# Kernel tuning notes

Hardware: AMD Instinct MI355X
Metric: run time of the kernel (lower is better)

The kernel has to match this reference:

```python
import jax, jax.numpy as jnp
import numpy as np
import math

D_MODEL = 1024
NUM_NEURONS = 2048
LUT_SIZE = 4096
TWO_PI = 2.0 * math.pi


def lut_sin_cos(theta, sin_table, cos_table):
    # Interpolated periodic table lookup over [0, 2*pi)
    n = sin_table.shape[0]
    pos = (theta / TWO_PI) * n
    pos = jnp.mod(pos, n)
    i0 = jnp.floor(pos).astype(jnp.int32)
    frac = pos - i0.astype(theta.dtype)
    i1 = jnp.mod(i0 + 1, n)
    s = sin_table[i0] * (1.0 - frac) + sin_table[i1] * frac
    c = cos_table[i0] * (1.0 - frac) + cos_table[i1] * frac
    return s, c


def setup_inputs() -> dict:
    key = jax.random.key(0)
    ks = jax.random.split(key, 10)
    B = 64
    x_real = jax.random.normal(ks[0], (B, D_MODEL), jnp.float32)
    x_imag = jax.random.normal(ks[1], (B, D_MODEL), jnp.float32)
    t = jax.random.uniform(ks[2], (B,), jnp.float32)
    # xavier_uniform with gain=0.5 for linear weights
    def xavier(k, shape, gain):
        fan_out, fan_in = shape
        a = gain * math.sqrt(6.0 / (fan_in + fan_out))
        return jax.random.uniform(k, shape, jnp.float32, -a, a)
    ic_w = xavier(ks[3], (D_MODEL, 2 * D_MODEL), 0.5)
    ic_b = jnp.zeros((D_MODEL,), jnp.float32)
    W = jax.random.normal(ks[4], (NUM_NEURONS, D_MODEL), jnp.float32) * 0.02
    Bp = jnp.zeros((NUM_NEURONS, D_MODEL), jnp.float32)
    attn_cos = jnp.ones((NUM_NEURONS, D_MODEL), jnp.float32)
    attn_sin = jnp.ones((NUM_NEURONS, D_MODEL), jnp.float32)
    wr = xavier(ks[5], (D_MODEL, NUM_NEURONS), 0.5)
    wi = xavier(ks[6], (D_MODEL, NUM_NEURONS), 0.5)
    grid = jnp.arange(LUT_SIZE, dtype=jnp.float32) * (TWO_PI / LUT_SIZE)
    sin_table = jnp.sin(grid)
    cos_table = jnp.cos(grid)
    return {"x_real": x_real, "x_imag": x_imag, "t": t,
            "ic_w": ic_w, "ic_b": ic_b, "W": W, "Bp": Bp,
            "attn_cos": attn_cos, "attn_sin": attn_sin,
            "wr": wr, "wi": wi,
            "sin_table": sin_table, "cos_table": cos_table}


def reference(x_real, x_imag, t, ic_w, ic_b, W, Bp, attn_cos, attn_sin, wr, wi, sin_table, cos_table):
    x_combined = jnp.concatenate([x_real, x_imag], axis=-1)          # [B, 2D]
    x_collapsed = x_combined @ ic_w.T + ic_b                          # [B, D]
    wavelength = 1.0 + jnp.abs(W)                                     # [N, D]
    theta = x_collapsed[:, None, :] / wavelength + Bp + t[:, None, None]  # [B, N, D]
    sin_t, cos_t = lut_sin_cos(theta, sin_table, cos_table)
    cos_sum = jnp.einsum('bnd,nd->bn', cos_t, attn_cos)               # fused weight+reduce
    sin_sum = jnp.einsum('bnd,nd->bn', sin_t, attn_sin)
    out_real = jax.nn.silu(cos_sum @ wr.T)                            # [B, D]
    out_imag = jax.nn.silu(sin_sum @ wi.T)
    return out_real, out_imag
```

## Files before the change

kernel.cpp:

```cpp
#include <hip/hip_runtime.h>
#include <stdint.h>

#define DM 1024
#define NN 2048
#define BB 64

static constexpr float INV2PI = 0.15915494309189535f;

__device__ __forceinline__ uint32_t bf16r(float x) {
  uint32_t b = __float_as_uint(x);
  b += 0x7fffu + ((b >> 16) & 1u);
  return b >> 16;
}

__global__ __launch_bounds__(256) void k0_prep(
    const float* __restrict__ xr, const float* __restrict__ xi,
    const float* __restrict__ W,
    float* __restrict__ xcombP, float* __restrict__ rinv)
{
  __shared__ float tile[64][65];
  int bid = blockIdx.x;
  int t = threadIdx.x;
  if (bid < 32) {
    int j = bid;
    int k0 = j * 64;
    const float* src = (k0 < 1024) ? xr : xi;
    int koff = k0 & 1023;
    int c = t & 63, rl = t >> 6;
#pragma unroll
    for (int i = 0; i < 16; ++i) {
      int b = rl * 16 + i;
      tile[b][c] = src[b * 1024 + koff + c];
    }
    __syncthreads();
    float2* out2 = (float2*)xcombP;
    int bl = t & 63, kp = t >> 6;
#pragma unroll
    for (int i = 0; i < 8; ++i) {
      int kl = (kp * 8 + i) * 2;
      float2 v = make_float2(tile[bl][kl], tile[bl][kl + 1]);
      out2[(size_t)((k0 + kl) >> 1) * 64 + bl] = v;
    }
  } else {
    int j = bid - 32;
    const float4* W4 = (const float4*)W;
    float4* R4 = (float4*)rinv;
    int base = j * 2048 + t;
#pragma unroll
    for (int i = 0; i < 8; ++i) {
      int idx = base + i * 256;
      float4 w = W4[idx];
      float4 r;
      r.x = 1.0f / (1.0f + fabsf(w.x));
      r.y = 1.0f / (1.0f + fabsf(w.y));
      r.z = 1.0f / (1.0f + fabsf(w.z));
      r.w = 1.0f / (1.0f + fabsf(w.w));
      R4[idx] = r;
    }
  }
}

__global__ __launch_bounds__(512) void k1_collapse(
    const float* __restrict__ xcombP, const float* __restrict__ icw,
    const float* __restrict__ icb, uint32_t* __restrict__ xcp)
{
  __shared__ float part[8][4][64];
  int d0 = blockIdx.x * 4;
  int wave = __builtin_amdgcn_readfirstlane((int)(threadIdx.x >> 6));
  int lane = threadIdx.x & 63;
  const float2* P2 = (const float2*)xcombP;
  float acc[4] = {0.f, 0.f, 0.f, 0.f};
  int kbase = wave * 256;
  for (int kk = 0; kk < 256; kk += 4) {
    int k = kbase + kk;
    float2 xa = P2[(size_t)(k >> 1) * 64 + lane];
    float2 xb = P2[(size_t)((k >> 1) + 1) * 64 + lane];
#pragma unroll
    for (int r = 0; r < 4; ++r) {
      float4 w = *(const float4*)(icw + (size_t)(d0 + r) * 2048 + k);
      acc[r] = fmaf(w.x, xa.x, acc[r]);
      acc[r] = fmaf(w.y, xa.y, acc[r]);
      acc[r] = fmaf(w.z, xb.x, acc[r]);
      acc[r] = fmaf(w.w, xb.y, acc[r]);
    }
  }
#pragma unroll
  for (int r = 0; r < 4; ++r) part[wave][r][lane] = acc[r];
  __syncthreads();
  int t = threadIdx.x;
  if (t < 128) {
    int pj = t >> 6;
    int b = t & 63;
    float s0 = 0.f, s1 = 0.f;
#pragma unroll
    for (int w = 0; w < 8; ++w) {
      s0 += part[w][2 * pj][b];
      s1 += part[w][2 * pj + 1][b];
    }
    float x0 = (s0 + icb[d0 + 2 * pj]) * INV2PI;
    float x1 = (s1 + icb[d0 + 2 * pj + 1]) * INV2PI;
    uint32_t u = bf16r(x0) | (bf16r(x1) << 16);
    xcp[(size_t)((d0 >> 1) + pj) * 64 + b] = u;
  }
}

#define K2_STEP(r4, b4, a4, s4, xu0, xu1)                                 \
  do {                                                                     \
    float x0 = __uint_as_float((xu0) << 16);                               \
    float x1 = __uint_as_float((xu0) & 0xffff0000u);                       \
    float x2 = __uint_as_float((xu1) << 16);                               \
    float x3 = __uint_as_float((xu1) & 0xffff0000u);                       \
    float rv0 = fmaf(x0, (r4).x, fmaf((b4).x, INV2PI, t2));                \
    accc0 = fmaf(__builtin_amdgcn_cosf(rv0), (a4).x, accc0);               \
    accs0 = fmaf(__builtin_amdgcn_sinf(rv0), (s4).x, accs0);               \
    float rv1 = fmaf(x1, (r4).y, fmaf((b4).y, INV2PI, t2));                \
    accc1 = fmaf(__builtin_amdgcn_cosf(rv1), (a4).y, accc1);               \
    accs1 = fmaf(__builtin_amdgcn_sinf(rv1), (s4).y, accs1);               \
    float rv2 = fmaf(x2, (r4).z, fmaf((b4).z, INV2PI, t2));                \
    accc0 = fmaf(__builtin_amdgcn_cosf(rv2), (a4).z, accc0);               \
    accs0 = fmaf(__builtin_amdgcn_sinf(rv2), (s4).z, accs0);               \
    float rv3 = fmaf(x3, (r4).w, fmaf((b4).w, INV2PI, t2));                \
    accc1 = fmaf(__builtin_amdgcn_cosf(rv3), (a4).w, accc1);               \
    accs1 = fmaf(__builtin_amdgcn_sinf(rv3), (s4).w, accs1);               \
  } while (0)

__global__ __launch_bounds__(512) void k2_resonant(
    const uint32_t* __restrict__ xcp, const float* __restrict__ rinv,
    const float* __restrict__ Bp, const float* __restrict__ ac,
    const float* __restrict__ as_, const float* __restrict__ tin,
    float* __restrict__ csP, float* __restrict__ ssP)
{
  __shared__ __align__(16) uint32_t xlds[64][64];
  __shared__ __align__(16) float plds[2][8][4][64];
  int wave = __builtin_amdgcn_readfirstlane((int)(threadIdx.x >> 6));
  int lane = threadIdx.x & 63;
  int bid = blockIdx.x;
  int q = bid & 7;
  int n = (bid >> 3) * 8 + wave;
  float t2 = tin[lane] * INV2PI;

  const char* xsrc = (const char*)(xcp + (size_t)q * 64 * 64);
  char* xdst = (char*)&xlds[0][0];
#pragma unroll
  for (int r = 0; r < 2; ++r) {
    int j = wave * 2 + r;
    __builtin_amdgcn_global_load_lds(
        (const __attribute__((address_space(1))) void*)(xsrc + j * 1024 + lane * 16),
        (__attribute__((address_space(3))) void*)(xdst + j * 1024), 16, 0, 0);
  }

  int g = lane >> 4;
  const float* ab = (g == 0) ? rinv : (g == 1) ? Bp : (g == 2) ? ac : as_;
  const float* gp = ab + (size_t)n * 1024 + (size_t)q * 128 + (lane & 15) * 4;
#pragma unroll
  for (int c = 0; c < 2; ++c) {
    __builtin_amdgcn_global_load_lds(
        (const __attribute__((address_space(1))) void*)(gp + c * 64),
        (__attribute__((address_space(3))) void*)&plds[c][wave][0][0], 16, 0, 0);
  }

  __syncthreads();

  float accc0 = 0.f, accs0 = 0.f, accc1 = 0.f, accs1 = 0.f;

#pragma unroll
  for (int c = 0; c < 2; ++c) {
    const float4* pr = (const float4*)&plds[c][wave][0][0];
#pragma unroll 4
    for (int i = 0; i < 16; ++i) {
      int ga = c * 16 + i;
      uint32_t xu0 = xlds[2 * ga][lane];
      uint32_t xu1 = xlds[2 * ga + 1][lane];
      float4 r4 = pr[i];
      float4 b4 = pr[16 + i];
      float4 a4 = pr[32 + i];
      float4 s4 = pr[48 + i];
      K2_STEP(r4, b4, a4, s4, xu0, xu1);
    }
  }

  size_t o = ((size_t)q * 2048 + n) * 64 + lane;
  csP[o] = accc0 + accc1;
  ssP[o] = accs0 + accs1;
}

__global__ __launch_bounds__(256) void k2b_reduce(
    const float* __restrict__ csP, const float* __restrict__ ssP,
    float* __restrict__ csT, float* __restrict__ ssT)
{
  int i = blockIdx.x * 256 + threadIdx.x;
  float c = 0.f, s = 0.f;
#pragma unroll
  for (int j = 0; j < 8; ++j) {
    c += csP[i + j * 131072];
    s += ssP[i + j * 131072];
  }
  csT[i] = c;
  ssT[i] = s;
}

__global__ __launch_bounds__(512) void k3_out(
    const float* __restrict__ csT, const float* __restrict__ ssT,
    const float* __restrict__ wr, const float* __restrict__ wi,
    float* __restrict__ out)
{
  __shared__ float part[8][4][65];
  int bid = blockIdx.x;
  int sel = bid >> 8;
  int d0 = (bid & 255) * 4;
  int wave = __builtin_amdgcn_readfirstlane((int)(threadIdx.x >> 6));
  int lane = threadIdx.x & 63;
  const float* src = sel ? ssT : csT;
  const float* wt = sel ? wi : wr;
  float acc[4] = {0.f, 0.f, 0.f, 0.f};
  int n0 = wave * 256;
  for (int i = 0; i < 64; ++i) {
    int n = n0 + i * 4;
    float cv0 = src[(size_t)(n + 0) * 64 + lane];
    float cv1 = src[(size_t)(n + 1) * 64 + lane];
    float cv2 = src[(size_t)(n + 2) * 64 + lane];
    float cv3 = src[(size_t)(n + 3) * 64 + lane];
#pragma unroll
    for (int r = 0; r < 4; ++r) {
      float4 wv = *(const float4*)(wt + (size_t)(d0 + r) * 2048 + n);
      acc[r] = fmaf(cv0, wv.x, acc[r]);
      acc[r] = fmaf(cv1, wv.y, acc[r]);
      acc[r] = fmaf(cv2, wv.z, acc[r]);
      acc[r] = fmaf(cv3, wv.w, acc[r]);
    }
  }
#pragma unroll
  for (int r = 0; r < 4; ++r) part[wave][r][lane] = acc[r];
  __syncthreads();
  int t = threadIdx.x;
  if (t < 256) {
    int b = t >> 2, j = t & 3;
    float s = 0.f;
#pragma unroll
    for (int w = 0; w < 8; ++w) s += part[w][j][b];
    float y = s / (1.0f + __expf(-s));
    out[(size_t)sel * 65536 + (size_t)b * 1024 + d0 + j] = y;
  }
}

extern "C" void kernel_launch(void* const* d_in, const int* in_sizes, int n_in,
                              void* d_out, int out_size, void* d_ws, size_t ws_size,
                              hipStream_t stream) {
  const float* xr  = (const float*)d_in[0];
  const float* xi  = (const float*)d_in[1];
  const float* t   = (const float*)d_in[2];
  const float* icw = (const float*)d_in[3];
  const float* icb = (const float*)d_in[4];
  const float* W   = (const float*)d_in[5];
  const float* Bp  = (const float*)d_in[6];
  const float* ac  = (const float*)d_in[7];
  const float* as_ = (const float*)d_in[8];
  const float* wr  = (const float*)d_in[9];
  const float* wi  = (const float*)d_in[10];

  float* ws = (float*)d_ws;
  float* rinv   = ws;
  float* xcombP = ws + 2097152;
  uint32_t* xcp = (uint32_t*)(ws + 2228224);
  float* csP    = ws + 2260992;
  float* ssP    = ws + 3309568;
  float* csT    = ws + 4358144;
  float* ssT    = ws + 4489216;
  float* out = (float*)d_out;

  k0_prep<<<dim3(288), dim3(256), 0, stream>>>(xr, xi, W, xcombP, rinv);
  k1_collapse<<<dim3(256), dim3(512), 0, stream>>>(xcombP, icw, icb, xcp);
  k2_resonant<<<dim3(2048), dim3(512), 0, stream>>>(xcp, rinv, Bp, ac, as_, t, csP, ssP);
  k2b_reduce<<<dim3(512), dim3(256), 0, stream>>>(csP, ssP, csT, ssT);
  k3_out<<<dim3(512), dim3(512), 0, stream>>>(csT, ssT, wr, wi, out);
}
```

Before: 78.20 us.

## Batch loads in collapse/output GEMVs, split k2 accumulators, pack reduced sums as bf16

k1_collapse and k3_out now issue 16 weight float4 loads and 8 activation loads per iteration before the FMAs, so more memory requests are in flight at once. k2_resonant is fully unrolled and uses four independent accumulator pairs, which shortens the FMA dependency chains. k2b_reduce now sums two neurons per thread and writes the results as packed bf16, halving the bytes k3_out reads for its activations. In exchange this adds bf16 rounding error on the reduced sums and raises register pressure in the unrolled loops.

```diff
diff --git a/kernel.cpp b/kernel.cpp
--- a/kernel.cpp
+++ b/kernel.cpp
@@ -71,17 +71,27 @@
   const float2* P2 = (const float2*)xcombP;
   float acc[4] = {0.f, 0.f, 0.f, 0.f};
   int kbase = wave * 256;
-  for (int kk = 0; kk < 256; kk += 4) {
+  for (int kk = 0; kk < 256; kk += 16) {
     int k = kbase + kk;
-    float2 xa = P2[(size_t)(k >> 1) * 64 + lane];
-    float2 xb = P2[(size_t)((k >> 1) + 1) * 64 + lane];
-#pragma unroll
-    for (int r = 0; r < 4; ++r) {
-      float4 w = *(const float4*)(icw + (size_t)(d0 + r) * 2048 + k);
-      acc[r] = fmaf(w.x, xa.x, acc[r]);
-      acc[r] = fmaf(w.y, xa.y, acc[r]);
-      acc[r] = fmaf(w.z, xb.x, acc[r]);
-      acc[r] = fmaf(w.w, xb.y, acc[r]);
+    float4 w[4][4];
+#pragma unroll
+    for (int r = 0; r < 4; ++r)
+#pragma unroll
+      for (int j = 0; j < 4; ++j)
+        w[r][j] = *(const float4*)(icw + (size_t)(d0 + r) * 2048 + k + 4 * j);
+    float2 xv[8];
+#pragma unroll
+    for (int j = 0; j < 8; ++j)
+      xv[j] = P2[(size_t)((k >> 1) + j) * 64 + lane];
+#pragma unroll
+    for (int j = 0; j < 4; ++j) {
+#pragma unroll
+      for (int r = 0; r < 4; ++r) {
+        acc[r] = fmaf(w[r][j].x, xv[2 * j].x, acc[r]);
+        acc[r] = fmaf(w[r][j].y, xv[2 * j].y, acc[r]);
+        acc[r] = fmaf(w[r][j].z, xv[2 * j + 1].x, acc[r]);
+        acc[r] = fmaf(w[r][j].w, xv[2 * j + 1].y, acc[r]);
+      }
     }
   }
 #pragma unroll
@@ -104,24 +114,24 @@
   }
 }
 
-#define K2_STEP(r4, b4, a4, s4, xu0, xu1)                                 \
+#define K2_STEP(r4, b4, a4, s4, xu0, xu1, AC0, AS0, AC1, AS1)              \
   do {                                                                     \
     float x0 = __uint_as_float((xu0) << 16);                               \
     float x1 = __uint_as_float((xu0) & 0xffff0000u);                       \
     float x2 = __uint_as_float((xu1) << 16);                               \
     float x3 = __uint_as_float((xu1) & 0xffff0000u);                       \
     float rv0 = fmaf(x0, (r4).x, fmaf((b4).x, INV2PI, t2));                \
-    accc0 = fmaf(__builtin_amdgcn_cosf(rv0), (a4).x, accc0);               \
-    accs0 = fmaf(__builtin_amdgcn_sinf(rv0), (s4).x, accs0);               \
+    AC0 = fmaf(__builtin_amdgcn_cosf(rv0), (a4).x, AC0);                   \
+    AS0 = fmaf(__builtin_amdgcn_sinf(rv0), (s4).x, AS0);                   \
     float rv1 = fmaf(x1, (r4).y, fmaf((b4).y, INV2PI, t2));                \
-    accc1 = fmaf(__builtin_amdgcn_cosf(rv1), (a4).y, accc1);               \
-    accs1 = fmaf(__builtin_amdgcn_sinf(rv1), (s4).y, accs1);               \
+    AC1 = fmaf(__builtin_amdgcn_cosf(rv1), (a4).y, AC1);                   \
+    AS1 = fmaf(__builtin_amdgcn_sinf(rv1), (s4).y, AS1);                   \
     float rv2 = fmaf(x2, (r4).z, fmaf((b4).z, INV2PI, t2));                \
-    accc0 = fmaf(__builtin_amdgcn_cosf(rv2), (a4).z, accc0);               \
-    accs0 = fmaf(__builtin_amdgcn_sinf(rv2), (s4).z, accs0);               \
+    AC0 = fmaf(__builtin_amdgcn_cosf(rv2), (a4).z, AC0);                   \
+    AS0 = fmaf(__builtin_amdgcn_sinf(rv2), (s4).z, AS0);                   \
     float rv3 = fmaf(x3, (r4).w, fmaf((b4).w, INV2PI, t2));                \
-    accc1 = fmaf(__builtin_amdgcn_cosf(rv3), (a4).w, accc1);               \
-    accs1 = fmaf(__builtin_amdgcn_sinf(rv3), (s4).w, accs1);               \
+    AC1 = fmaf(__builtin_amdgcn_cosf(rv3), (a4).w, AC1);                   \
+    AS1 = fmaf(__builtin_amdgcn_sinf(rv3), (s4).w, AS1);                   \
   } while (0)
 
 __global__ __launch_bounds__(512) void k2_resonant(
@@ -161,46 +171,63 @@
 
   __syncthreads();
 
-  float accc0 = 0.f, accs0 = 0.f, accc1 = 0.f, accs1 = 0.f;
-
-#pragma unroll
-  for (int c = 0; c < 2; ++c) {
-    const float4* pr = (const float4*)&plds[c][wave][0][0];
-#pragma unroll 4
+  float ac0 = 0.f, as0 = 0.f, ac1 = 0.f, as1 = 0.f;
+  float ac2 = 0.f, as2 = 0.f, ac3 = 0.f, as3 = 0.f;
+
+  {
+    const float4* pr = (const float4*)&plds[0][wave][0][0];
+#pragma unroll
     for (int i = 0; i < 16; ++i) {
-      int ga = c * 16 + i;
-      uint32_t xu0 = xlds[2 * ga][lane];
-      uint32_t xu1 = xlds[2 * ga + 1][lane];
+      uint32_t xu0 = xlds[2 * i][lane];
+      uint32_t xu1 = xlds[2 * i + 1][lane];
       float4 r4 = pr[i];
       float4 b4 = pr[16 + i];
       float4 a4 = pr[32 + i];
       float4 s4 = pr[48 + i];
-      K2_STEP(r4, b4, a4, s4, xu0, xu1);
+      K2_STEP(r4, b4, a4, s4, xu0, xu1, ac0, as0, ac1, as1);
+    }
+  }
+  {
+    const float4* pr = (const float4*)&plds[1][wave][0][0];
+#pragma unroll
+    for (int i = 0; i < 16; ++i) {
+      uint32_t xu0 = xlds[32 + 2 * i][lane];
+      uint32_t xu1 = xlds[32 + 2 * i + 1][lane];
+      float4 r4 = pr[i];
+      float4 b4 = pr[16 + i];
+      float4 a4 = pr[32 + i];
+      float4 s4 = pr[48 + i];
+      K2_STEP(r4, b4, a4, s4, xu0, xu1, ac2, as2, ac3, as3);
     }
   }
 
   size_t o = ((size_t)q * 2048 + n) * 64 + lane;
-  csP[o] = accc0 + accc1;
-  ssP[o] = accs0 + accs1;
+  csP[o] = (ac0 + ac1) + (ac2 + ac3);
+  ssP[o] = (as0 + as1) + (as2 + as3);
 }
 
 __global__ __launch_bounds__(256) void k2b_reduce(
     const float* __restrict__ csP, const float* __restrict__ ssP,
-    float* __restrict__ csT, float* __restrict__ ssT)
+    uint32_t* __restrict__ csB, uint32_t* __restrict__ ssB)
 {
   int i = blockIdx.x * 256 + threadIdx.x;
-  float c = 0.f, s = 0.f;
+  int np = i >> 6, b = i & 63;
+  int n0 = 2 * np;
+  float c0 = 0.f, c1 = 0.f, s0 = 0.f, s1 = 0.f;
 #pragma unroll
   for (int j = 0; j < 8; ++j) {
-    c += csP[i + j * 131072];
-    s += ssP[i + j * 131072];
-  }
-  csT[i] = c;
-  ssT[i] = s;
+    size_t base = ((size_t)j * 2048 + n0) * 64 + b;
+    c0 += csP[base];
+    c1 += csP[base + 64];
+    s0 += ssP[base];
+    s1 += ssP[base + 64];
+  }
+  csB[i] = bf16r(c0) | (bf16r(c1) << 16);
+  ssB[i] = bf16r(s0) | (bf16r(s1) << 16);
 }
 
 __global__ __launch_bounds__(512) void k3_out(
-    const float* __restrict__ csT, const float* __restrict__ ssT,
+    const uint32_t* __restrict__ csB, const uint32_t* __restrict__ ssB,
     const float* __restrict__ wr, const float* __restrict__ wi,
     float* __restrict__ out)
 {
@@ -210,23 +237,40 @@
   int d0 = (bid & 255) * 4;
   int wave = __builtin_amdgcn_readfirstlane((int)(threadIdx.x >> 6));
   int lane = threadIdx.x & 63;
-  const float* src = sel ? ssT : csT;
+  const uint32_t* src2 = sel ? ssB : csB;
   const float* wt = sel ? wi : wr;
   float acc[4] = {0.f, 0.f, 0.f, 0.f};
   int n0 = wave * 256;
-  for (int i = 0; i < 64; ++i) {
-    int n = n0 + i * 4;
-    float cv0 = src[(size_t)(n + 0) * 64 + lane];
-    float cv1 = src[(size_t)(n + 1) * 64 + lane];
-    float cv2 = src[(size_t)(n + 2) * 64 + lane];
-    float cv3 = src[(size_t)(n + 3) * 64 + lane];
-#pragma unroll
-    for (int r = 0; r < 4; ++r) {
-      float4 wv = *(const float4*)(wt + (size_t)(d0 + r) * 2048 + n);
-      acc[r] = fmaf(cv0, wv.x, acc[r]);
-      acc[r] = fmaf(cv1, wv.y, acc[r]);
-      acc[r] = fmaf(cv2, wv.z, acc[r]);
-      acc[r] = fmaf(cv3, wv.w, acc[r]);
+  for (int i = 0; i < 16; ++i) {
+    int n = n0 + i * 16;
+    float4 w[4][4];
+#pragma unroll
+    for (int r = 0; r < 4; ++r)
+#pragma unroll
+      for (int j = 0; j < 4; ++j)
+        w[r][j] = *(const float4*)(wt + (size_t)(d0 + r) * 2048 + n + 4 * j);
+    uint32_t xu[8];
+#pragma unroll
+    for (int j = 0; j < 8; ++j)
+      xu[j] = src2[(size_t)((n >> 1) + j) * 64 + lane];
+#pragma unroll
+    for (int j = 0; j < 8; ++j) {
+      float cv0 = __uint_as_float(xu[j] << 16);
+      float cv1 = __uint_as_float(xu[j] & 0xffff0000u);
+      const int q4 = j >> 1;
+      if ((j & 1) == 0) {
+#pragma unroll
+        for (int r = 0; r < 4; ++r) {
+          acc[r] = fmaf(cv0, w[r][q4].x, acc[r]);
+          acc[r] = fmaf(cv1, w[r][q4].y, acc[r]);
+        }
+      } else {
+#pragma unroll
+        for (int r = 0; r < 4; ++r) {
+          acc[r] = fmaf(cv0, w[r][q4].z, acc[r]);
+          acc[r] = fmaf(cv1, w[r][q4].w, acc[r]);
+        }
+      }
     }
   }
 #pragma unroll
@@ -264,13 +308,13 @@
   uint32_t* xcp = (uint32_t*)(ws + 2228224);
   float* csP    = ws + 2260992;
   float* ssP    = ws + 3309568;
-  float* csT    = ws + 4358144;
-  float* ssT    = ws + 4489216;
+  uint32_t* csB = (uint32_t*)(ws + 4358144);
+  uint32_t* ssB = (uint32_t*)(ws + 4423680);
   float* out = (float*)d_out;
 
   k0_prep<<<dim3(288), dim3(256), 0, stream>>>(xr, xi, W, xcombP, rinv);
   k1_collapse<<<dim3(256), dim3(512), 0, stream>>>(xcombP, icw, icb, xcp);
   k2_resonant<<<dim3(2048), dim3(512), 0, stream>>>(xcp, rinv, Bp, ac, as_, t, csP, ssP);
-  k2b_reduce<<<dim3(512), dim3(256), 0, stream>>>(csP, ssP, csT, ssT);
-  k3_out<<<dim3(512), dim3(512), 0, stream>>>(csT, ssT, wr, wi, out);
-}
+  k2b_reduce<<<dim3(256), dim3(256), 0, stream>>>(csP, ssP, csB, ssB);
+  k3_out<<<dim3(512), dim3(512), 0, stream>>>(csB, ssB, wr, wi, out);
+}
```

Result: slower. 93.17 us (+19.1%).
